# Performance work log

Hardware: AMD Instinct MI355X
Metric: run time of the kernel (lower is better)

## Reference

```python
import math
import jax, jax.numpy as jnp
import numpy as np

B, N, D = 32, 1025, 768
K, CD, TD = 64, 128, 256  # num_clusters, cluster_dim, token_dim
REG = 0.1
NUM_ITERS = 5


def setup_inputs() -> dict:
    key = jax.random.key(0)
    ks = jax.random.split(key, 8)
    x = jax.random.normal(ks[0], (B, N, D), dtype=jnp.float32)
    # Linear params (torch nn.Linear: y = x @ W.T + b; we store W already transposed as [in, out])
    Wf = jax.random.normal(ks[1], (D, CD), dtype=jnp.float32) / math.sqrt(D)
    bf = jnp.zeros((CD,), dtype=jnp.float32)
    Ws = jax.random.normal(ks[2], (D, K), dtype=jnp.float32) / math.sqrt(D)
    bs = jnp.zeros((K,), dtype=jnp.float32)
    Wt = jax.random.normal(ks[3], (D, TD), dtype=jnp.float32) / math.sqrt(D)
    bt = jnp.zeros((TD,), dtype=jnp.float32)
    anchors = jax.random.normal(ks[4], (K, CD), dtype=jnp.float32) * 0.1
    dust_bin = jnp.float32(1.0)
    sharpness = jnp.float32(5.0)
    return {"x": x, "Wf": Wf, "bf": bf, "Ws": Ws, "bs": bs, "Wt": Wt, "bt": bt,
            "anchors": anchors, "dust_bin": dust_bin, "sharpness": sharpness}


def _log_otp_solver(log_a, log_b, M, num_iters, reg):
    M = M / reg
    u = jnp.zeros_like(log_a)  # [B, K+1]
    v = jnp.zeros_like(log_b)  # [B, N-1]
    for _ in range(num_iters):
        u = log_a - jax.nn.logsumexp(M + v[:, None, :], axis=2)
        v = log_b - jax.nn.logsumexp(M + u[:, :, None], axis=1)
    return M + u[:, :, None] + v[:, None, :]


def reference(x, Wf, bf, Ws, bs, Wt, bt, anchors, dust_bin, sharpness):
    b, n, d = x.shape
    t_global = x[:, 0]            # [B, D]
    fi = x[:, 1:]                 # [B, N-1, D]
    f = fi @ Wf + bf              # [B, N-1, CD]
    s = jnp.swapaxes(fi @ Ws + bs, 1, 2)  # [B, K, N-1]
    t = t_global @ Wt + bt        # [B, TD]
    s = s * sharpness
    dust = jnp.broadcast_to(dust_bin, (b, 1, n - 1))
    s_aug = jnp.concatenate([s, dust], axis=1)  # [B, K+1, N-1]
    log_a = jnp.full((b, K + 1), -math.log(K + 1), dtype=x.dtype)
    log_b = jnp.full((b, n - 1), -math.log(n - 1), dtype=x.dtype)
    log_P = _log_otp_solver(log_a, log_b, s_aug, NUM_ITERS, REG)
    p = jnp.exp(log_P)[:, :-1, :]  # [B, K, N-1]
    # v_agg = sum_n p[b,k,n] * (2*f[b,n,:] - anchors[k,:])  (algebraic rewrite of the broadcast sum)
    v_agg = 2.0 * jnp.einsum('bkn,bnc->bkc', p, f) - p.sum(axis=2)[:, :, None] * anchors[None]
    v_local = v_agg.reshape(b, -1)            # [B, K*CD]
    f_out = jnp.concatenate([t, v_local], axis=-1)
    norm = jnp.maximum(jnp.linalg.norm(f_out, axis=-1, keepdims=True), 1e-12)
    return f_out / norm
```

## Files before the change

kernel.cpp:

```cpp
#include <hip/hip_runtime.h>
#include <math.h>


#define BATCH 32
#define NTOK  1025
#define DIM   768
#define KDIM  64
#define CDIM  128
#define TDIM  256
#define NM1   1024
#define ROWLEN 8448
#define NITER 5
#define INV_REG 10.0f
#define NS_AGG 8
#define LOG_A (-4.17438727f)
#define LOG_B (-6.93147181f)

typedef __attribute__((ext_vector_type(8))) short short8;
typedef __attribute__((ext_vector_type(4))) float floatx4;

typedef __attribute__((address_space(3))) unsigned int lds_uint;
typedef const __attribute__((address_space(1))) unsigned int glb_uint;

__device__ __forceinline__ void gload_lds16(const void* g, void* l) {
    __builtin_amdgcn_global_load_lds((glb_uint*)g, (lds_uint*)l, 16, 0, 0);
}

__device__ __forceinline__ unsigned short bf16_rne(float f) {
    unsigned u = __builtin_bit_cast(unsigned, f);
    unsigned r = u + 0x7FFFu + ((u >> 16) & 1u);
    return (unsigned short)(r >> 16);
}

__device__ __forceinline__ short8 cvt8(float4 a, float4 b) {
    short8 r;
    r[0] = (short)bf16_rne(a.x); r[1] = (short)bf16_rne(a.y);
    r[2] = (short)bf16_rne(a.z); r[3] = (short)bf16_rne(a.w);
    r[4] = (short)bf16_rne(b.x); r[5] = (short)bf16_rne(b.y);
    r[6] = (short)bf16_rne(b.z); r[7] = (short)bf16_rne(b.w);
    return r;
}

__global__ __launch_bounds__(256) void prep(
    const float* __restrict__ Wf, const float* __restrict__ Ws,
    const float* __restrict__ bf, const float* __restrict__ bs,
    const float* __restrict__ x, const float* __restrict__ Wt,
    short* __restrict__ W_pack, float* __restrict__ bias_all,
    float* __restrict__ tpart)
{
    __shared__ float xr[256];
    const int blk = blockIdx.x, tid = threadIdx.x;
    if (blk < 576) {
        int idx = blk * 256 + tid;
        int g    = idx / 6144;
        int rem  = idx - g * 6144;
        int nf   = rem >> 9;
        int rem2 = rem & 511;
        int lane = rem2 >> 3;
        int j    = rem2 & 7;
        int k = g * 32 + (lane >> 4) * 8 + j;
        int c = nf * 16 + (lane & 15);
        float v = (c < CDIM) ? Wf[(size_t)k * CDIM + c] : Ws[(size_t)k * KDIM + (c - CDIM)];
        W_pack[idx] = (short)bf16_rne(v);
        if (idx < 192) bias_all[idx] = (idx < CDIM) ? bf[idx] : bs[idx - CDIM];
    } else {
        int i = blk - 576;
        int b = i / 3, dy = i - b * 3;
        xr[tid] = x[(size_t)b * NTOK * DIM + (size_t)dy * 256 + tid];
        __syncthreads();
        float acc = 0.f;
        const float* wp = Wt + (size_t)dy * 256 * TDIM + tid;
#pragma unroll 8
        for (int d = 0; d < 256; ++d) acc = fmaf(xr[d], wp[(size_t)d * TDIM], acc);
        tpart[((size_t)dy * BATCH + b) * TDIM + tid] = acc;
    }
}

__global__ __launch_bounds__(256, 2) void gemm_fs(
    const float* __restrict__ x, const short* __restrict__ W_pack,
    const float* __restrict__ bias_all, const float* __restrict__ sharp_p,
    unsigned short* __restrict__ fT, float* __restrict__ Mmat)
{
    __shared__ __align__(16) short Bs[12288];
    __shared__ __align__(16) short As[4096];
    const int tid  = threadIdx.x;
    const int wave = tid >> 6, lane = tid & 63;
    const int quad = lane >> 4, lrow = lane & 15;
    const int R = blockIdx.x * 64 + wave * 16;

    const int arow = blockIdx.x * 64 + (tid >> 2);
    const float* asrc = x + ((size_t)(arow >> 10) * NTOK + 1 + (arow & 1023)) * DIM + (tid & 3) * 16;
    const int r    = (tid >> 2) & 15;
    const int seg  = tid & 3;
    const int kk_w = seg >> 1;
    const int q0   = (seg & 1) * 2;
    short* adst0 = &As[(((tid >> 6) * 2 + kk_w) * 64 + q0 * 16 + r) * 8];
    short* adst1 = &As[(((tid >> 6) * 2 + kk_w) * 64 + (q0 + 1) * 16 + r) * 8];

    floatx4 acc[12];
#pragma unroll
    for (int nf = 0; nf < 12; ++nf) acc[nf] = (floatx4){0.f, 0.f, 0.f, 0.f};

    float4 g0 = *(const float4*)(asrc);
    float4 g1 = *(const float4*)(asrc + 4);
    float4 g2 = *(const float4*)(asrc + 8);
    float4 g3 = *(const float4*)(asrc + 12);

    for (int ko = 0; ko < 12; ++ko) {
        __syncthreads();
        const short* bsrc = W_pack + ko * 12288 + tid * 8;
#pragma unroll
        for (int i = 0; i < 6; ++i)
            gload_lds16(bsrc + i * 2048, &Bs[i * 2048 + tid * 8]);
        *(short8*)adst0 = cvt8(g0, g1);
        *(short8*)adst1 = cvt8(g2, g3);
        if (ko < 11) {
            const float* ap = asrc + (ko + 1) * 64;
            g0 = *(const float4*)(ap);
            g1 = *(const float4*)(ap + 4);
            g2 = *(const float4*)(ap + 8);
            g3 = *(const float4*)(ap + 12);
        }
        __syncthreads();
#pragma unroll
        for (int kk = 0; kk < 2; ++kk) {
            short8 af = *(const short8*)&As[((wave * 2 + kk) * 64 + lane) * 8];
#pragma unroll
            for (int nf = 0; nf < 12; ++nf) {
                short8 bf8 = *(const short8*)&Bs[((kk * 12 + nf) * 64 + lane) * 8];
                acc[nf] = __builtin_amdgcn_mfma_f32_16x16x32_bf16(af, bf8, acc[nf], 0, 0, 0);
            }
        }
    }

    const float sc = sharp_p[0] * INV_REG;
    const int bb = R >> 10;
    const int tok = (R & 1023) + quad * 4;
#pragma unroll
    for (int nf = 0; nf < 12; ++nf) {
        const int c = nf * 16 + lrow;
        const float bias = bias_all[c];
        if (nf < 8) {
            ushort4 w;
            w.x = bf16_rne(acc[nf][0] + bias);
            w.y = bf16_rne(acc[nf][1] + bias);
            w.z = bf16_rne(acc[nf][2] + bias);
            w.w = bf16_rne(acc[nf][3] + bias);
            *(ushort4*)(fT + ((size_t)bb * CDIM + c) * NM1 + tok) = w;
        } else {
            const int k = c - CDIM;
            float4 w = make_float4((acc[nf][0] + bias) * sc, (acc[nf][1] + bias) * sc,
                                   (acc[nf][2] + bias) * sc, (acc[nf][3] + bias) * sc);
            *(float4*)(Mmat + ((size_t)bb * KDIM + k) * NM1 + tok) = w;
        }
    }
}

template<bool FIRST>
__global__ __launch_bounds__(256) void sink_u(
    const float* __restrict__ Mmat, const float* __restrict__ v_in,
    const float* __restrict__ dust_p, float* __restrict__ u_out)
{
    const int wv   = (blockIdx.x << 2) + (threadIdx.x >> 6);
    const int lane = threadIdx.x & 63;
    const int b = wv / 65, k = wv - b * 65;
    const float dustM = dust_p[0] * INV_REG;

    const float4* vp = (const float4*)(v_in + (size_t)b * NM1);
    float xs[16];
    if (k < 64) {
        const float4* Mp = (const float4*)(Mmat + ((size_t)b * KDIM + k) * NM1);
#pragma unroll
        for (int i = 0; i < 4; ++i) {
            float4 mv = Mp[i * 64 + lane];
            float4 vv = FIRST ? make_float4(0.f, 0.f, 0.f, 0.f) : vp[i * 64 + lane];
            xs[i * 4 + 0] = mv.x + vv.x;
            xs[i * 4 + 1] = mv.y + vv.y;
            xs[i * 4 + 2] = mv.z + vv.z;
            xs[i * 4 + 3] = mv.w + vv.w;
        }
    } else {
#pragma unroll
        for (int i = 0; i < 4; ++i) {
            float4 vv = FIRST ? make_float4(0.f, 0.f, 0.f, 0.f) : vp[i * 64 + lane];
            xs[i * 4 + 0] = dustM + vv.x;
            xs[i * 4 + 1] = dustM + vv.y;
            xs[i * 4 + 2] = dustM + vv.z;
            xs[i * 4 + 3] = dustM + vv.w;
        }
    }
    float m = xs[0];
#pragma unroll
    for (int i = 1; i < 16; ++i) m = fmaxf(m, xs[i]);
#pragma unroll
    for (int off = 1; off < 64; off <<= 1) m = fmaxf(m, __shfl_xor(m, off));
    float S = 0.f;
#pragma unroll
    for (int i = 0; i < 16; ++i) S += __expf(xs[i] - m);
#pragma unroll
    for (int off = 1; off < 64; off <<= 1) S += __shfl_xor(S, off);
    if (lane == 0) u_out[wv] = LOG_A - (m + __logf(S));
}

__global__ __launch_bounds__(128) void sink_v(
    const float* __restrict__ Mmat, const float* __restrict__ u_in,
    const float* __restrict__ dust_p, float* __restrict__ v_out)
{
    __shared__ float us[65];
    const int b = blockIdx.x, tid = threadIdx.x;
    const int n = blockIdx.y * 128 + tid;
    if (tid < 65) us[tid] = u_in[b * 65 + tid];
    __syncthreads();
    const float* Mb = Mmat + (size_t)b * KDIM * NM1 + n;
    float xs[64];
#pragma unroll
    for (int k = 0; k < 64; ++k) xs[k] = Mb[(size_t)k * NM1] + us[k];
    const float xd = dust_p[0] * INV_REG + us[64];
    float m = xd;
#pragma unroll
    for (int k = 0; k < 64; ++k) m = fmaxf(m, xs[k]);
    float S = __expf(xd - m);
#pragma unroll
    for (int k = 0; k < 64; ++k) S += __expf(xs[k] - m);
    v_out[(size_t)b * NM1 + n] = LOG_B - (m + __logf(S));
}

__global__ __launch_bounds__(256) void aggregate(
    const float* __restrict__ Mmat, const unsigned short* __restrict__ fT,
    const float* __restrict__ u_in, const float* __restrict__ v_in,
    float* __restrict__ vpart, float* __restrict__ rspart)
{
    __shared__ float us[KDIM];
    __shared__ float vsh[128];
    const int b = blockIdx.x, ns = blockIdx.y;
    const int tid = threadIdx.x;
    const int wave = tid >> 6, lane = tid & 63;
    const int quad = lane >> 4, lrow = lane & 15;

    if (tid < 64) us[tid] = u_in[b * 65 + tid];
    else if (tid < 192) vsh[tid - 64] = v_in[(size_t)b * NM1 + ns * 128 + (tid - 64)];
    __syncthreads();

    const int krow = wave * 16 + lrow;
    const float uk = us[krow];
    const float* Mrow = Mmat + ((size_t)b * KDIM + krow) * NM1 + ns * 128 + quad * 8;
    const unsigned short* fbase = fT + ((size_t)b * CDIM + lrow) * NM1 + ns * 128 + quad * 8;

    floatx4 acc[8];
#pragma unroll
    for (int nf = 0; nf < 8; ++nf) acc[nf] = (floatx4){0.f, 0.f, 0.f, 0.f};
    float rs = 0.f;

#pragma unroll
    for (int step = 0; step < 4; ++step) {
        const float* mp = Mrow + step * 32;
        float4 m0 = *(const float4*)(mp);
        float4 m1 = *(const float4*)(mp + 4);
        const int tb = step * 32 + quad * 8;
        float p[8];
        p[0] = __expf(m0.x + uk + vsh[tb + 0]);
        p[1] = __expf(m0.y + uk + vsh[tb + 1]);
        p[2] = __expf(m0.z + uk + vsh[tb + 2]);
        p[3] = __expf(m0.w + uk + vsh[tb + 3]);
        p[4] = __expf(m1.x + uk + vsh[tb + 4]);
        p[5] = __expf(m1.y + uk + vsh[tb + 5]);
        p[6] = __expf(m1.z + uk + vsh[tb + 6]);
        p[7] = __expf(m1.w + uk + vsh[tb + 7]);
        short8 afrag;
#pragma unroll
        for (int j = 0; j < 8; ++j) {
            rs += p[j];
            afrag[j] = (short)bf16_rne(p[j]);
        }
#pragma unroll
        for (int nf = 0; nf < 8; ++nf) {
            short8 bfrag = *(const short8*)(fbase + (size_t)nf * 16 * NM1 + step * 32);
            acc[nf] = __builtin_amdgcn_mfma_f32_16x16x32_bf16(afrag, bfrag, acc[nf], 0, 0, 0);
        }
    }

    rs += __shfl_xor(rs, 16);
    rs += __shfl_xor(rs, 32);
    if (lane < 16) rspart[(ns * BATCH + b) * KDIM + krow] = rs;

    float* vp = vpart + (size_t)(ns * BATCH + b) * (KDIM * CDIM);
#pragma unroll
    for (int nf = 0; nf < 8; ++nf) {
        const int c = nf * 16 + lrow;
#pragma unroll
        for (int j = 0; j < 4; ++j)
            vp[(size_t)(wave * 16 + quad * 4 + j) * CDIM + c] = acc[nf][j];
    }
}

__global__ __launch_bounds__(1024) void finalize_all(
    const float* __restrict__ vpart, const float* __restrict__ rspart,
    const float* __restrict__ anchors, const float* __restrict__ tpart,
    const float* __restrict__ bt, float* __restrict__ out)
{
    __shared__ float rstot[KDIM];
    __shared__ float red[16];
    __shared__ float sc_sh;
    const int b = blockIdx.x, tid = threadIdx.x;
    const int lane = tid & 63, wave = tid >> 6;

    if (tid < KDIM) {
        float s = 0.f;
#pragma unroll
        for (int ns = 0; ns < NS_AGG; ++ns)
            s += rspart[(ns * BATCH + b) * KDIM + tid];
        rstot[tid] = s;
    }
    __syncthreads();

    const size_t e0 = (size_t)tid * 8;
    float4 s0 = make_float4(0.f, 0.f, 0.f, 0.f);
    float4 s1 = make_float4(0.f, 0.f, 0.f, 0.f);
#pragma unroll
    for (int ns = 0; ns < NS_AGG; ++ns) {
        const float* vp = vpart + (size_t)(ns * BATCH + b) * (KDIM * CDIM) + e0;
        float4 a = *(const float4*)(vp);
        float4 c = *(const float4*)(vp + 4);
        s0.x += a.x; s0.y += a.y; s0.z += a.z; s0.w += a.w;
        s1.x += c.x; s1.y += c.y; s1.z += c.z; s1.w += c.w;
    }
    const float rsv = rstot[tid >> 4];
    float4 a0 = *(const float4*)(anchors + e0);
    float4 a1 = *(const float4*)(anchors + e0 + 4);
    float4 v0, v1;
    v0.x = 2.f * s0.x - rsv * a0.x;  v0.y = 2.f * s0.y - rsv * a0.y;
    v0.z = 2.f * s0.z - rsv * a0.z;  v0.w = 2.f * s0.w - rsv * a0.w;
    v1.x = 2.f * s1.x - rsv * a1.x;  v1.y = 2.f * s1.y - rsv * a1.y;
    v1.z = 2.f * s1.z - rsv * a1.z;  v1.w = 2.f * s1.w - rsv * a1.w;
    float ss = v0.x*v0.x + v0.y*v0.y + v0.z*v0.z + v0.w*v0.w
             + v1.x*v1.x + v1.y*v1.y + v1.z*v1.z + v1.w*v1.w;

    float t = 0.f;
    if (tid < TDIM) {
        t = bt[tid];
#pragma unroll
        for (int s = 0; s < 3; ++s) t += tpart[((size_t)s * BATCH + b) * TDIM + tid];
        ss += t * t;
    }

#pragma unroll
    for (int off = 32; off > 0; off >>= 1) ss += __shfl_down(ss, off);
    if (lane == 0) red[wave] = ss;
    __syncthreads();
    if (tid == 0) {
        float tot = 0.f;
#pragma unroll
        for (int i = 0; i < 16; ++i) tot += red[i];
        sc_sh = 1.f / fmaxf(sqrtf(tot), 1e-12f);
    }
    __syncthreads();
    const float scale = sc_sh;

    float* orow = out + (size_t)b * ROWLEN;
    if (tid < TDIM) orow[tid] = t * scale;
    v0.x *= scale; v0.y *= scale; v0.z *= scale; v0.w *= scale;
    v1.x *= scale; v1.y *= scale; v1.z *= scale; v1.w *= scale;
    *(float4*)&orow[TDIM + e0]     = v0;
    *(float4*)&orow[TDIM + e0 + 4] = v1;
}

extern "C" void kernel_launch(void* const* d_in, const int* in_sizes, int n_in,
                              void* d_out, int out_size, void* d_ws, size_t ws_size,
                              hipStream_t stream)
{
    const float* x       = (const float*)d_in[0];
    const float* Wf      = (const float*)d_in[1];
    const float* bf      = (const float*)d_in[2];
    const float* Ws      = (const float*)d_in[3];
    const float* bs      = (const float*)d_in[4];
    const float* Wt      = (const float*)d_in[5];
    const float* bt      = (const float*)d_in[6];
    const float* anchors = (const float*)d_in[7];
    const float* dust    = (const float*)d_in[8];
    const float* sharp   = (const float*)d_in[9];
    float* out = (float*)d_out;

    char* base = (char*)d_ws;
    short* W_pack        = (short*)base;
    float* bias_all      = (float*)(base + 294912);
    float* Mmat          = bias_all + 192;
    unsigned short* fT   = (unsigned short*)(Mmat + (size_t)BATCH * KDIM * NM1);
    float* u_buf         = (float*)(fT + (size_t)BATCH * CDIM * NM1);
    float* v_buf         = u_buf + BATCH * 65;
    float* vpart         = v_buf + BATCH * NM1;
    float* rspart        = vpart + (size_t)NS_AGG * BATCH * KDIM * CDIM;
    float* tpart         = rspart + NS_AGG * BATCH * KDIM;

    hipLaunchKernelGGL(prep, dim3(672), dim3(256), 0, stream,
                       Wf, Ws, bf, bs, x, Wt, W_pack, bias_all, tpart);
    hipLaunchKernelGGL(gemm_fs, dim3(512), dim3(256), 0, stream,
                       x, W_pack, bias_all, sharp, fT, Mmat);

    hipLaunchKernelGGL(HIP_KERNEL_NAME(sink_u<true>), dim3(520), dim3(256), 0, stream,
                       Mmat, v_buf, dust, u_buf);
    hipLaunchKernelGGL(sink_v, dim3(BATCH, 8), dim3(128), 0, stream,
                       Mmat, u_buf, dust, v_buf);
    for (int it = 1; it < NITER; ++it) {
        hipLaunchKernelGGL(HIP_KERNEL_NAME(sink_u<false>), dim3(520), dim3(256), 0, stream,
                           Mmat, v_buf, dust, u_buf);
        hipLaunchKernelGGL(sink_v, dim3(BATCH, 8), dim3(128), 0, stream,
                           Mmat, u_buf, dust, v_buf);
    }

    hipLaunchKernelGGL(aggregate, dim3(BATCH, NS_AGG), dim3(256), 0, stream,
                       Mmat, fT, u_buf, v_buf, vpart, rspart);
    hipLaunchKernelGGL(finalize_all, dim3(BATCH), dim3(1024), 0, stream,
                       vpart, rspart, anchors, tpart, bt, out);
}
```

Baseline: 242.2 us.

## Fuse Sinkhorn iterations into one cooperative kernel with LDS-resident cost matrix

Replaces the ten alternating sink_u/sink_v launches with a single cooperative kernel of 64 blocks, two per batch. Each block keeps its half of the cost matrix in 128 KB of LDS and exchanges partial logsumexp (max, sum) pairs for u through global memory, using grid syncs between iterations. This removes repeated launch overhead and repeated global reads of the matrix. In exchange it runs on only 64 workgroups, depends on 128 KB of LDS per block being available, and adds grid-wide barriers.

After: 402.7 us. 1.66x slower.

```diff
diff --git a/kernel.cpp b/kernel.cpp
--- a/kernel.cpp
+++ b/kernel.cpp
@@ -1,4 +1,5 @@
 #include <hip/hip_runtime.h>
+#include <hip/hip_cooperative_groups.h>
 #include <math.h>
 
 
@@ -156,73 +157,121 @@
     }
 }
 
-template<bool FIRST>
-__global__ __launch_bounds__(256) void sink_u(
-    const float* __restrict__ Mmat, const float* __restrict__ v_in,
-    const float* __restrict__ dust_p, float* __restrict__ u_out)
-{
-    const int wv   = (blockIdx.x << 2) + (threadIdx.x >> 6);
-    const int lane = threadIdx.x & 63;
-    const int b = wv / 65, k = wv - b * 65;
+__device__ __forceinline__ void u_partial(
+    const float* Msh, const float* vs, float* upp, int blk,
+    int wave, int lane, float dustM, bool use_v)
+{
+#pragma unroll
+    for (int r = 0; r < 4; ++r) {
+        const int k = wave * 4 + r;
+        float loc[8];
+        float m = -INFINITY;
+#pragma unroll
+        for (int i = 0; i < 8; ++i) {
+            float xv = Msh[k * 512 + i * 64 + lane] + (use_v ? vs[i * 64 + lane] : 0.f);
+            loc[i] = xv;
+            m = fmaxf(m, xv);
+        }
+#pragma unroll
+        for (int off = 1; off < 64; off <<= 1) m = fmaxf(m, __shfl_xor(m, off));
+        float S = 0.f;
+#pragma unroll
+        for (int i = 0; i < 8; ++i) S += __expf(loc[i] - m);
+#pragma unroll
+        for (int off = 1; off < 64; off <<= 1) S += __shfl_xor(S, off);
+        if (lane == 0) {
+            upp[(blk * 65 + k) * 2]     = m;
+            upp[(blk * 65 + k) * 2 + 1] = S;
+        }
+    }
+    if (wave == 0) {
+        float m, S;
+        if (use_v) {
+            float loc[8];
+            float vm = -INFINITY;
+#pragma unroll
+            for (int i = 0; i < 8; ++i) { loc[i] = vs[i * 64 + lane]; vm = fmaxf(vm, loc[i]); }
+#pragma unroll
+            for (int off = 1; off < 64; off <<= 1) vm = fmaxf(vm, __shfl_xor(vm, off));
+            float s = 0.f;
+#pragma unroll
+            for (int i = 0; i < 8; ++i) s += __expf(loc[i] - vm);
+#pragma unroll
+            for (int off = 1; off < 64; off <<= 1) s += __shfl_xor(s, off);
+            m = dustM + vm; S = s;
+        } else {
+            m = dustM; S = 512.f;
+        }
+        if (lane == 0) {
+            upp[(blk * 65 + 64) * 2]     = m;
+            upp[(blk * 65 + 64) * 2 + 1] = S;
+        }
+    }
+}
+
+__global__ __launch_bounds__(1024) void sink_coop(
+    const float* __restrict__ Mmat, const float* __restrict__ dust_p,
+    float* __restrict__ u_buf, float* __restrict__ v_buf,
+    float* __restrict__ up)
+{
+    extern __shared__ float Msh[];
+    __shared__ float us[65];
+    __shared__ float vs[512];
+    cooperative_groups::grid_group grid = cooperative_groups::this_grid();
+    const int blk = blockIdx.x, b = blk >> 1, h = blk & 1;
+    const int tid = threadIdx.x, wave = tid >> 6, lane = tid & 63;
     const float dustM = dust_p[0] * INV_REG;
 
-    const float4* vp = (const float4*)(v_in + (size_t)b * NM1);
-    float xs[16];
-    if (k < 64) {
-        const float4* Mp = (const float4*)(Mmat + ((size_t)b * KDIM + k) * NM1);
-#pragma unroll
-        for (int i = 0; i < 4; ++i) {
-            float4 mv = Mp[i * 64 + lane];
-            float4 vv = FIRST ? make_float4(0.f, 0.f, 0.f, 0.f) : vp[i * 64 + lane];
-            xs[i * 4 + 0] = mv.x + vv.x;
-            xs[i * 4 + 1] = mv.y + vv.y;
-            xs[i * 4 + 2] = mv.z + vv.z;
-            xs[i * 4 + 3] = mv.w + vv.w;
-        }
-    } else {
-#pragma unroll
-        for (int i = 0; i < 4; ++i) {
-            float4 vv = FIRST ? make_float4(0.f, 0.f, 0.f, 0.f) : vp[i * 64 + lane];
-            xs[i * 4 + 0] = dustM + vv.x;
-            xs[i * 4 + 1] = dustM + vv.y;
-            xs[i * 4 + 2] = dustM + vv.z;
-            xs[i * 4 + 3] = dustM + vv.w;
-        }
-    }
-    float m = xs[0];
-#pragma unroll
-    for (int i = 1; i < 16; ++i) m = fmaxf(m, xs[i]);
-#pragma unroll
-    for (int off = 1; off < 64; off <<= 1) m = fmaxf(m, __shfl_xor(m, off));
-    float S = 0.f;
-#pragma unroll
-    for (int i = 0; i < 16; ++i) S += __expf(xs[i] - m);
-#pragma unroll
-    for (int off = 1; off < 64; off <<= 1) S += __shfl_xor(S, off);
-    if (lane == 0) u_out[wv] = LOG_A - (m + __logf(S));
-}
-
-__global__ __launch_bounds__(128) void sink_v(
-    const float* __restrict__ Mmat, const float* __restrict__ u_in,
-    const float* __restrict__ dust_p, float* __restrict__ v_out)
-{
-    __shared__ float us[65];
-    const int b = blockIdx.x, tid = threadIdx.x;
-    const int n = blockIdx.y * 128 + tid;
-    if (tid < 65) us[tid] = u_in[b * 65 + tid];
+    {
+        const float4* src = (const float4*)(Mmat + (size_t)b * KDIM * NM1 + h * 512);
+        float4* dst = (float4*)Msh;
+#pragma unroll
+        for (int q = 0; q < 8; ++q) {
+            int idx = q * 1024 + tid;
+            int k = idx >> 7, j4 = idx & 127;
+            dst[k * 128 + j4] = src[(size_t)k * 256 + j4];
+        }
+    }
     __syncthreads();
-    const float* Mb = Mmat + (size_t)b * KDIM * NM1 + n;
-    float xs[64];
-#pragma unroll
-    for (int k = 0; k < 64; ++k) xs[k] = Mb[(size_t)k * NM1] + us[k];
-    const float xd = dust_p[0] * INV_REG + us[64];
-    float m = xd;
-#pragma unroll
-    for (int k = 0; k < 64; ++k) m = fmaxf(m, xs[k]);
-    float S = __expf(xd - m);
-#pragma unroll
-    for (int k = 0; k < 64; ++k) S += __expf(xs[k] - m);
-    v_out[(size_t)b * NM1 + n] = LOG_B - (m + __logf(S));
+
+    u_partial(Msh, vs, up, blk, wave, lane, dustM, false);
+    __threadfence();
+    grid.sync();
+
+    for (int it = 0; it < NITER; ++it) {
+        const float* rd = up + (it & 1) * (64 * 65 * 2);
+        if (tid < 65) {
+            const int peer = blk ^ 1;
+            float m0 = rd[(blk * 65 + tid) * 2],  S0 = rd[(blk * 65 + tid) * 2 + 1];
+            float m1 = rd[(peer * 65 + tid) * 2], S1 = rd[(peer * 65 + tid) * 2 + 1];
+            float mm = fmaxf(m0, m1);
+            float S = S0 * __expf(m0 - mm) + S1 * __expf(m1 - mm);
+            us[tid] = LOG_A - (mm + __logf(S));
+        }
+        __syncthreads();
+        if (tid < 512) {
+            float xs[64];
+#pragma unroll
+            for (int k = 0; k < 64; ++k) xs[k] = Msh[k * 512 + tid] + us[k];
+            const float xd = dustM + us[64];
+            float m = xd;
+#pragma unroll
+            for (int k = 0; k < 64; ++k) m = fmaxf(m, xs[k]);
+            float S = __expf(xd - m);
+#pragma unroll
+            for (int k = 0; k < 64; ++k) S += __expf(xs[k] - m);
+            vs[tid] = LOG_B - (m + __logf(S));
+        }
+        __syncthreads();
+        if (it < NITER - 1) {
+            u_partial(Msh, vs, up + ((it + 1) & 1) * (64 * 65 * 2), blk, wave, lane, dustM, true);
+            __threadfence();
+            grid.sync();
+        } else {
+            if (h == 0 && tid < 65) u_buf[b * 65 + tid] = us[tid];
+            if (tid < 512) v_buf[(size_t)b * NM1 + h * 512 + tid] = vs[tid];
+        }
+    }
 }
 
 __global__ __launch_bounds__(256) void aggregate(
@@ -390,21 +439,25 @@
     float* vpart         = v_buf + BATCH * NM1;
     float* rspart        = vpart + (size_t)NS_AGG * BATCH * KDIM * CDIM;
     float* tpart         = rspart + NS_AGG * BATCH * KDIM;
+    float* up            = tpart + 3 * BATCH * TDIM;
 
     hipLaunchKernelGGL(prep, dim3(672), dim3(256), 0, stream,
                        Wf, Ws, bf, bs, x, Wt, W_pack, bias_all, tpart);
     hipLaunchKernelGGL(gemm_fs, dim3(512), dim3(256), 0, stream,
                        x, W_pack, bias_all, sharp, fT, Mmat);
 
-    hipLaunchKernelGGL(HIP_KERNEL_NAME(sink_u<true>), dim3(520), dim3(256), 0, stream,
-                       Mmat, v_buf, dust, u_buf);
-    hipLaunchKernelGGL(sink_v, dim3(BATCH, 8), dim3(128), 0, stream,
-                       Mmat, u_buf, dust, v_buf);
-    for (int it = 1; it < NITER; ++it) {
-        hipLaunchKernelGGL(HIP_KERNEL_NAME(sink_u<false>), dim3(520), dim3(256), 0, stream,
-                           Mmat, v_buf, dust, u_buf);
-        hipLaunchKernelGGL(sink_v, dim3(BATCH, 8), dim3(128), 0, stream,
-                           Mmat, u_buf, dust, v_buf);
+    {
+        static bool attr_set = false;
+        if (!attr_set) {
+            hipFuncSetAttribute(reinterpret_cast<const void*>(sink_coop),
+                                hipFuncAttributeMaxDynamicSharedMemorySize, 131072);
+            attr_set = true;
+        }
+        const float* Mc = Mmat; const float* dc = dust;
+        float* ub = u_buf; float* vb = v_buf; float* upp = up;
+        void* args[] = { (void*)&Mc, (void*)&dc, (void*)&ub, (void*)&vb, (void*)&upp };
+        hipLaunchCooperativeKernel(reinterpret_cast<void*>(sink_coop),
+                                   dim3(64), dim3(1024), args, 131072, stream);
     }
 
     hipLaunchKernelGGL(aggregate, dim3(BATCH, NS_AGG), dim3(256), 0, stream,
```

## Fuse Sinkhorn u/v steps into tiled kernel with partial logsumexp merging

Applied to the files above, without the earlier changes.

Replaces the alternating sink_u/sink_v launches with a single per-(batch, token-slice) kernel. Each launch stages a 64x128 M tile in LDS, computes v for its slice, then emits per-slice partial (max, sum) pairs for the next u update. The next launch merges these pairs online to recover u. The final iteration fuses the v step with the aggregation MFMA, and the first u step uses v=0 with a closed-form dust row. This cuts kernel launches from about eleven to six and avoids rereading M for separate u passes, at the cost of lower parallelism (256 blocks) and 32KB of LDS per block.

Measured after the change: 261.7 us. 1.08x slower.

```diff
diff --git a/kernel.cpp b/kernel.cpp
--- a/kernel.cpp
+++ b/kernel.cpp
@@ -156,38 +156,26 @@
     }
 }
 
-template<bool FIRST>
-__global__ __launch_bounds__(256) void sink_u(
-    const float* __restrict__ Mmat, const float* __restrict__ v_in,
-    const float* __restrict__ dust_p, float* __restrict__ u_out)
+__global__ __launch_bounds__(256) void sink_u0(
+    const float* __restrict__ Mmat, const float* __restrict__ dust_p,
+    float* __restrict__ u_out)
 {
     const int wv   = (blockIdx.x << 2) + (threadIdx.x >> 6);
     const int lane = threadIdx.x & 63;
     const int b = wv / 65, k = wv - b * 65;
     const float dustM = dust_p[0] * INV_REG;
 
-    const float4* vp = (const float4*)(v_in + (size_t)b * NM1);
+    if (k == 64) {
+        if (lane == 0) u_out[wv] = LOG_A - (dustM + 6.93147181f);
+        return;
+    }
+    const float4* Mp = (const float4*)(Mmat + ((size_t)b * KDIM + k) * NM1);
     float xs[16];
-    if (k < 64) {
-        const float4* Mp = (const float4*)(Mmat + ((size_t)b * KDIM + k) * NM1);
-#pragma unroll
-        for (int i = 0; i < 4; ++i) {
-            float4 mv = Mp[i * 64 + lane];
-            float4 vv = FIRST ? make_float4(0.f, 0.f, 0.f, 0.f) : vp[i * 64 + lane];
-            xs[i * 4 + 0] = mv.x + vv.x;
-            xs[i * 4 + 1] = mv.y + vv.y;
-            xs[i * 4 + 2] = mv.z + vv.z;
-            xs[i * 4 + 3] = mv.w + vv.w;
-        }
-    } else {
-#pragma unroll
-        for (int i = 0; i < 4; ++i) {
-            float4 vv = FIRST ? make_float4(0.f, 0.f, 0.f, 0.f) : vp[i * 64 + lane];
-            xs[i * 4 + 0] = dustM + vv.x;
-            xs[i * 4 + 1] = dustM + vv.y;
-            xs[i * 4 + 2] = dustM + vv.z;
-            xs[i * 4 + 3] = dustM + vv.w;
-        }
+#pragma unroll
+    for (int i = 0; i < 4; ++i) {
+        float4 mv = Mp[i * 64 + lane];
+        xs[i * 4 + 0] = mv.x; xs[i * 4 + 1] = mv.y;
+        xs[i * 4 + 2] = mv.z; xs[i * 4 + 3] = mv.w;
     }
     float m = xs[0];
 #pragma unroll
@@ -202,94 +190,141 @@
     if (lane == 0) u_out[wv] = LOG_A - (m + __logf(S));
 }
 
-__global__ __launch_bounds__(128) void sink_v(
-    const float* __restrict__ Mmat, const float* __restrict__ u_in,
-    const float* __restrict__ dust_p, float* __restrict__ v_out)
-{
+template<bool FIRST, bool LAST>
+__global__ __launch_bounds__(256) void sink_step(
+    const float* __restrict__ Mmat, const float* __restrict__ dust_p,
+    const float* __restrict__ u_in, float* __restrict__ up_out,
+    const unsigned short* __restrict__ fT,
+    float* __restrict__ vpart, float* __restrict__ rspart)
+{
+    __shared__ float Msh[KDIM * 128];
     __shared__ float us[65];
-    const int b = blockIdx.x, tid = threadIdx.x;
-    const int n = blockIdx.y * 128 + tid;
-    if (tid < 65) us[tid] = u_in[b * 65 + tid];
-    __syncthreads();
-    const float* Mb = Mmat + (size_t)b * KDIM * NM1 + n;
-    float xs[64];
-#pragma unroll
-    for (int k = 0; k < 64; ++k) xs[k] = Mb[(size_t)k * NM1] + us[k];
-    const float xd = dust_p[0] * INV_REG + us[64];
-    float m = xd;
-#pragma unroll
-    for (int k = 0; k < 64; ++k) m = fmaxf(m, xs[k]);
-    float S = __expf(xd - m);
-#pragma unroll
-    for (int k = 0; k < 64; ++k) S += __expf(xs[k] - m);
-    v_out[(size_t)b * NM1 + n] = LOG_B - (m + __logf(S));
-}
-
-__global__ __launch_bounds__(256) void aggregate(
-    const float* __restrict__ Mmat, const unsigned short* __restrict__ fT,
-    const float* __restrict__ u_in, const float* __restrict__ v_in,
-    float* __restrict__ vpart, float* __restrict__ rspart)
-{
-    __shared__ float us[KDIM];
-    __shared__ float vsh[128];
+    __shared__ float vs[128];
     const int b = blockIdx.x, ns = blockIdx.y;
     const int tid = threadIdx.x;
     const int wave = tid >> 6, lane = tid & 63;
-    const int quad = lane >> 4, lrow = lane & 15;
-
-    if (tid < 64) us[tid] = u_in[b * 65 + tid];
-    else if (tid < 192) vsh[tid - 64] = v_in[(size_t)b * NM1 + ns * 128 + (tid - 64)];
+    const float dustM = dust_p[0] * INV_REG;
+
+    const float* msrc = Mmat + (size_t)b * KDIM * NM1 + ns * 128;
+#pragma unroll
+    for (int q = 0; q < 8; ++q) {
+        int idx = q * 256 + tid;
+        int k = idx >> 5, j4 = idx & 31;
+        *(float4*)&Msh[k * 128 + j4 * 4] = *(const float4*)(msrc + (size_t)k * NM1 + j4 * 4);
+    }
+
+    if (tid < 65) {
+        if (FIRST) {
+            us[tid] = u_in[b * 65 + tid];
+        } else {
+            const float* pp = u_in + b * 1040 + tid * 16;
+            float m = pp[0], S = pp[1];
+#pragma unroll
+            for (int j = 1; j < 8; ++j) {
+                float m2 = pp[j * 2], S2 = pp[j * 2 + 1];
+                float nm = fmaxf(m, m2);
+                S = S * __expf(m - nm) + S2 * __expf(m2 - nm);
+                m = nm;
+            }
+            us[tid] = LOG_A - (m + __logf(S));
+        }
+    }
     __syncthreads();
 
-    const int krow = wave * 16 + lrow;
-    const float uk = us[krow];
-    const float* Mrow = Mmat + ((size_t)b * KDIM + krow) * NM1 + ns * 128 + quad * 8;
-    const unsigned short* fbase = fT + ((size_t)b * CDIM + lrow) * NM1 + ns * 128 + quad * 8;
-
-    floatx4 acc[8];
-#pragma unroll
-    for (int nf = 0; nf < 8; ++nf) acc[nf] = (floatx4){0.f, 0.f, 0.f, 0.f};
-    float rs = 0.f;
-
-#pragma unroll
-    for (int step = 0; step < 4; ++step) {
-        const float* mp = Mrow + step * 32;
-        float4 m0 = *(const float4*)(mp);
-        float4 m1 = *(const float4*)(mp + 4);
-        const int tb = step * 32 + quad * 8;
-        float p[8];
-        p[0] = __expf(m0.x + uk + vsh[tb + 0]);
-        p[1] = __expf(m0.y + uk + vsh[tb + 1]);
-        p[2] = __expf(m0.z + uk + vsh[tb + 2]);
-        p[3] = __expf(m0.w + uk + vsh[tb + 3]);
-        p[4] = __expf(m1.x + uk + vsh[tb + 4]);
-        p[5] = __expf(m1.y + uk + vsh[tb + 5]);
-        p[6] = __expf(m1.z + uk + vsh[tb + 6]);
-        p[7] = __expf(m1.w + uk + vsh[tb + 7]);
-        short8 afrag;
-#pragma unroll
-        for (int j = 0; j < 8; ++j) {
-            rs += p[j];
-            afrag[j] = (short)bf16_rne(p[j]);
-        }
+    if (tid < 128) {
+        float xs[64];
+#pragma unroll
+        for (int k = 0; k < 64; ++k) xs[k] = Msh[k * 128 + tid] + us[k];
+        const float xd = dustM + us[64];
+        float m = xd;
+#pragma unroll
+        for (int k = 0; k < 64; ++k) m = fmaxf(m, xs[k]);
+        float S = __expf(xd - m);
+#pragma unroll
+        for (int k = 0; k < 64; ++k) S += __expf(xs[k] - m);
+        vs[tid] = LOG_B - (m + __logf(S));
+    }
+    __syncthreads();
+
+    if (!LAST) {
+#pragma unroll 4
+        for (int r = 0; r < 16; ++r) {
+            const int k = wave * 16 + r;
+            float x0 = Msh[k * 128 + lane] + vs[lane];
+            float x1 = Msh[k * 128 + 64 + lane] + vs[64 + lane];
+            float m = fmaxf(x0, x1);
+#pragma unroll
+            for (int off = 1; off < 64; off <<= 1) m = fmaxf(m, __shfl_xor(m, off));
+            float S = __expf(x0 - m) + __expf(x1 - m);
+#pragma unroll
+            for (int off = 1; off < 64; off <<= 1) S += __shfl_xor(S, off);
+            if (lane == 0)
+                *(float2*)&up_out[b * 1040 + k * 16 + ns * 2] = make_float2(m, S);
+        }
+        if (wave == 0) {
+            float x0 = dustM + vs[lane];
+            float x1 = dustM + vs[64 + lane];
+            float m = fmaxf(x0, x1);
+#pragma unroll
+            for (int off = 1; off < 64; off <<= 1) m = fmaxf(m, __shfl_xor(m, off));
+            float S = __expf(x0 - m) + __expf(x1 - m);
+#pragma unroll
+            for (int off = 1; off < 64; off <<= 1) S += __shfl_xor(S, off);
+            if (lane == 0)
+                *(float2*)&up_out[b * 1040 + 64 * 16 + ns * 2] = make_float2(m, S);
+        }
+    } else {
+        const int quad = lane >> 4, lrow = lane & 15;
+        const int krow = wave * 16 + lrow;
+        const float uk = us[krow];
+        const float* Mrow = Mmat + ((size_t)b * KDIM + krow) * NM1 + ns * 128 + quad * 8;
+        const unsigned short* fbase = fT + ((size_t)b * CDIM + lrow) * NM1 + ns * 128 + quad * 8;
+
+        floatx4 acc[8];
+#pragma unroll
+        for (int nf = 0; nf < 8; ++nf) acc[nf] = (floatx4){0.f, 0.f, 0.f, 0.f};
+        float rs = 0.f;
+
+#pragma unroll
+        for (int step = 0; step < 4; ++step) {
+            const float* mp = Mrow + step * 32;
+            float4 m0 = *(const float4*)(mp);
+            float4 m1 = *(const float4*)(mp + 4);
+            const int tb = step * 32 + quad * 8;
+            float p[8];
+            p[0] = __expf(m0.x + uk + vs[tb + 0]);
+            p[1] = __expf(m0.y + uk + vs[tb + 1]);
+            p[2] = __expf(m0.z + uk + vs[tb + 2]);
+            p[3] = __expf(m0.w + uk + vs[tb + 3]);
+            p[4] = __expf(m1.x + uk + vs[tb + 4]);
+            p[5] = __expf(m1.y + uk + vs[tb + 5]);
+            p[6] = __expf(m1.z + uk + vs[tb + 6]);
+            p[7] = __expf(m1.w + uk + vs[tb + 7]);
+            short8 afrag;
+#pragma unroll
+            for (int j = 0; j < 8; ++j) {
+                rs += p[j];
+                afrag[j] = (short)bf16_rne(p[j]);
+            }
+#pragma unroll
+            for (int nf = 0; nf < 8; ++nf) {
+                short8 bfrag = *(const short8*)(fbase + (size_t)nf * 16 * NM1 + step * 32);
+                acc[nf] = __builtin_amdgcn_mfma_f32_16x16x32_bf16(afrag, bfrag, acc[nf], 0, 0, 0);
+            }
+        }
+
+        rs += __shfl_xor(rs, 16);
+        rs += __shfl_xor(rs, 32);
+        if (lane < 16) rspart[(ns * BATCH + b) * KDIM + krow] = rs;
+
+        float* vp = vpart + (size_t)(ns * BATCH + b) * (KDIM * CDIM);
 #pragma unroll
         for (int nf = 0; nf < 8; ++nf) {
-            short8 bfrag = *(const short8*)(fbase + (size_t)nf * 16 * NM1 + step * 32);
-            acc[nf] = __builtin_amdgcn_mfma_f32_16x16x32_bf16(afrag, bfrag, acc[nf], 0, 0, 0);
-        }
-    }
-
-    rs += __shfl_xor(rs, 16);
-    rs += __shfl_xor(rs, 32);
-    if (lane < 16) rspart[(ns * BATCH + b) * KDIM + krow] = rs;
-
-    float* vp = vpart + (size_t)(ns * BATCH + b) * (KDIM * CDIM);
-#pragma unroll
-    for (int nf = 0; nf < 8; ++nf) {
-        const int c = nf * 16 + lrow;
-#pragma unroll
-        for (int j = 0; j < 4; ++j)
-            vp[(size_t)(wave * 16 + quad * 4 + j) * CDIM + c] = acc[nf][j];
+            const int c = nf * 16 + lrow;
+#pragma unroll
+            for (int j = 0; j < 4; ++j)
+                vp[(size_t)(wave * 16 + quad * 4 + j) * CDIM + c] = acc[nf][j];
+        }
     }
 }
 
@@ -386,8 +421,9 @@
     float* Mmat          = bias_all + 192;
     unsigned short* fT   = (unsigned short*)(Mmat + (size_t)BATCH * KDIM * NM1);
     float* u_buf         = (float*)(fT + (size_t)BATCH * CDIM * NM1);
-    float* v_buf         = u_buf + BATCH * 65;
-    float* vpart         = v_buf + BATCH * NM1;
+    float* upA           = u_buf + BATCH * 65;
+    float* upB           = upA + BATCH * 1040;
+    float* vpart         = upB + BATCH * 1040;
     float* rspart        = vpart + (size_t)NS_AGG * BATCH * KDIM * CDIM;
     float* tpart         = rspart + NS_AGG * BATCH * KDIM;
 
@@ -396,19 +432,19 @@
     hipLaunchKernelGGL(gemm_fs, dim3(512), dim3(256), 0, stream,
                        x, W_pack, bias_all, sharp, fT, Mmat);
 
-    hipLaunchKernelGGL(HIP_KERNEL_NAME(sink_u<true>), dim3(520), dim3(256), 0, stream,
-                       Mmat, v_buf, dust, u_buf);
-    hipLaunchKernelGGL(sink_v, dim3(BATCH, 8), dim3(128), 0, stream,
-                       Mmat, u_buf, dust, v_buf);
-    for (int it = 1; it < NITER; ++it) {
-        hipLaunchKernelGGL(HIP_KERNEL_NAME(sink_u<false>), dim3(520), dim3(256), 0, stream,
-                           Mmat, v_buf, dust, u_buf);
-        hipLaunchKernelGGL(sink_v, dim3(BATCH, 8), dim3(128), 0, stream,
-                           Mmat, u_buf, dust, v_buf);
-    }
-
-    hipLaunchKernelGGL(aggregate, dim3(BATCH, NS_AGG), dim3(256), 0, stream,
-                       Mmat, fT, u_buf, v_buf, vpart, rspart);
+    hipLaunchKernelGGL(sink_u0, dim3(520), dim3(256), 0, stream,
+                       Mmat, dust, u_buf);
+    hipLaunchKernelGGL(HIP_KERNEL_NAME(sink_step<true,  false>), dim3(BATCH, NS_AGG), dim3(256), 0, stream,
+                       Mmat, dust, u_buf, upA, fT, vpart, rspart);
+    hipLaunchKernelGGL(HIP_KERNEL_NAME(sink_step<false, false>), dim3(BATCH, NS_AGG), dim3(256), 0, stream,
+                       Mmat, dust, upA, upB, fT, vpart, rspart);
+    hipLaunchKernelGGL(HIP_KERNEL_NAME(sink_step<false, false>), dim3(BATCH, NS_AGG), dim3(256), 0, stream,
+                       Mmat, dust, upB, upA, fT, vpart, rspart);
+    hipLaunchKernelGGL(HIP_KERNEL_NAME(sink_step<false, false>), dim3(BATCH, NS_AGG), dim3(256), 0, stream,
+                       Mmat, dust, upA, upB, fT, vpart, rspart);
+    hipLaunchKernelGGL(HIP_KERNEL_NAME(sink_step<false, true >), dim3(BATCH, NS_AGG), dim3(256), 0, stream,
+                       Mmat, dust, upB, upA, fT, vpart, rspart);
+
     hipLaunchKernelGGL(finalize_all, dim3(BATCH), dim3(1024), 0, stream,
                        vpart, rspart, anchors, tpart, bt, out);
 }
```
